# Performance work log

Measured on AMD Instinct MI355X. Metric: run time of the kernel, lower is better.

The kernel has to match this reference:

```python
import jax, jax.numpy as jnp
import numpy as np

NEG_SLOPE = 0.01  # torch LeakyReLU default
MIN_FREQ = 1.0
MAX_FREQ = 10.0
W = 100
N_HIDDEN = 100
N_OBS = 64

def _leaky(x):
    return jnp.where(x >= 0, x, NEG_SLOPE * x)

def setup_inputs() -> dict:
    key = jax.random.key(0)
    ks = jax.random.split(key, 7)
    # kaiming_uniform-ish init scales (exact init doesn't matter for correctness baseline)
    def unif(k, shape, fan_in):
        bound = np.sqrt(6.0 / fan_in)
        return jax.random.uniform(k, shape, jnp.float32, -bound, bound)
    x = jax.random.normal(ks[0], (65536, N_OBS), jnp.float32)
    W_in = unif(ks[1], (N_OBS, W), N_OBS)
    b_in = jnp.zeros((W,), jnp.float32)
    Ws = unif(ks[2], (N_HIDDEN, W, W), W)
    bs = jnp.zeros((N_HIDDEN, W), jnp.float32)
    W_out = unif(ks[3], (W, 1), W)
    b_out = jnp.zeros((1,), jnp.float32)
    return {"x": x, "W_in": W_in, "b_in": b_in, "Ws": Ws, "bs": bs,
            "W_out": W_out, "b_out": b_out}

def reference(x, W_in, b_in, Ws, bs, W_out, b_out):
    h = _leaky(x @ W_in + b_in)                       # [B, 100]
    def layer(h, wb):
        w, b = wb
        return _leaky(h @ w + b), None
    h, _ = jax.lax.scan(layer, h, (Ws, bs))           # 100 hidden layers
    a = h @ W_out + b_out                             # [B, 1]
    a = jnp.tanh(a)
    return (a + 1.0) / 2.0 * (MAX_FREQ - MIN_FREQ) + MIN_FREQ
```

## Files before the change

### kernel.cpp

```cpp
#include <hip/hip_runtime.h>
#include <cmath>

#define NLAYERS 100
#define DIN     64
#define WDIM    100
#define NTT     8
#define NTW     4
#define RT      4
#define ROWS    64
#define PSTR    136
#define RTPLANE (16 * PSTR)
#define BUF     (RT * RTPLANE)

typedef _Float16 half8 __attribute__((ext_vector_type(8)));
typedef _Float16 half2v __attribute__((ext_vector_type(2)));
typedef __fp16   fp16x2 __attribute__((ext_vector_type(2)));
typedef float    f32x4 __attribute__((ext_vector_type(4)));

#define WSH_LAYER_HALVES (4 * NTT * 64 * 8)
#define WSH_HALVES       (NLAYERS * WSH_LAYER_HALVES)
#define W0_HALVES        (2 * NTT * 64 * 8)
#define BPAD_FLOATS      128
#define OFF_BPAD_B       ((WSH_HALVES + W0_HALVES) * 2)
#define OFF_WOUT_B       (OFF_BPAD_B + BPAD_FLOATS * 4)
#define WOUT_FLOATS      128
#define TOTAL_PREP       (WSH_HALVES + W0_HALVES + BPAD_FLOATS + WOUT_FLOATS)

__global__ void actor_prep(const float* __restrict__ Win, const float* __restrict__ bin,
                           const float* __restrict__ Ws,  const float* __restrict__ bs,
                           const float* __restrict__ Wout,
                           _Float16* __restrict__ wsh, _Float16* __restrict__ w0sh,
                           float* __restrict__ bpad, float* __restrict__ woutp) {
    int t = blockIdx.x * 256 + threadIdx.x;
    if (t < WSH_HALVES) {
        int j    = t & 7;
        int lane = (t >> 3) & 63;
        int fid  = t >> 9;
        int nt   = fid & 7;
        int r2   = fid >> 3;
        int ks   = r2 & 3;
        int l    = r2 >> 2;
        int k = ks * 32 + (lane >> 4) * 8 + j;
        int n = nt * 16 + (lane & 15);
        float v = 0.f;
        if (k < WDIM && n < WDIM)            v = Ws[(l * WDIM + k) * WDIM + n];
        else if (k == 112 && n < WDIM)       v = bs[l * WDIM + n];
        else if (k == 112 && n == 112)       v = 1.0f;
        wsh[t] = (_Float16)v;
        return;
    }
    int t2 = t - WSH_HALVES;
    if (t2 < W0_HALVES) {
        int j    = t2 & 7;
        int lane = (t2 >> 3) & 63;
        int fid  = t2 >> 9;
        int nt   = fid & 7;
        int ks   = fid >> 3;
        int k = ks * 32 + (lane >> 4) * 8 + j;
        int n = nt * 16 + (lane & 15);
        float v = (k < DIN && n < WDIM) ? Win[k * WDIM + n] : 0.f;
        w0sh[t2] = (_Float16)v;
        return;
    }
    int t3 = t2 - W0_HALVES;
    if (t3 < BPAD_FLOATS) {
        float v = (t3 < WDIM) ? bin[t3] : (t3 == 112 ? 1.0f : 0.f);
        bpad[t3] = v;
        return;
    }
    int t4 = t3 - BPAD_FLOATS;
    if (t4 < WOUT_FLOATS) woutp[t4] = (t4 < WDIM) ? Wout[t4] : 0.f;
}

__device__ __forceinline__ void split8(const float* __restrict__ p, half8& hi, half8& lo) {
    f32x4 u0 = *(const f32x4*)p;
    f32x4 u1 = *(const f32x4*)(p + 4);
    float v[8] = {u0[0], u0[1], u0[2], u0[3], u1[0], u1[1], u1[2], u1[3]};
#pragma unroll
    for (int e = 0; e < 8; e += 2) {
        fp16x2 h = __builtin_amdgcn_cvt_pkrtz(v[e], v[e + 1]);
        float r0 = v[e]     - (float)h[0];
        float r1 = v[e + 1] - (float)h[1];
        fp16x2 l = __builtin_amdgcn_cvt_pkrtz(r0, r1);
        hi[e] = (_Float16)h[0]; hi[e + 1] = (_Float16)h[1];
        lo[e] = (_Float16)l[0]; lo[e + 1] = (_Float16)l[1];
    }
}

__device__ __forceinline__ void ep_tile(const f32x4 a, _Float16* __restrict__ d) {
    half2v p01, p23;
    p01[0] = (_Float16)a[0]; p01[1] = (_Float16)a[1];
    p23[0] = (_Float16)a[2]; p23[1] = (_Float16)a[3];
    const half2v slope = {(_Float16)0.01f, (_Float16)0.01f};
    p01 = __builtin_elementwise_max(p01, p01 * slope);
    p23 = __builtin_elementwise_max(p23, p23 * slope);
    uint2 w;
    w.x = __builtin_bit_cast(unsigned, p01);
    w.y = __builtin_bit_cast(unsigned, p23);
    *reinterpret_cast<uint2*>(d) = w;
}

__global__ __launch_bounds__(128, 2)
void actor_main(const float* __restrict__ x,
                const _Float16* __restrict__ wsh,
                const _Float16* __restrict__ w0sh,
                const float* __restrict__ bpad,
                const float* __restrict__ woutp,
                const float* __restrict__ bout,
                float* __restrict__ out) {
    __shared__ _Float16 hp[2 * BUF];
    const int lane = threadIdx.x & 63;
    const int wid  = threadIdx.x >> 6;
    const int q = lane >> 4, l15 = lane & 15;
    const int rowbase = blockIdx.x * ROWS;
    const int ntb = wid * NTW;

    f32x4 acc[RT][NTW];
    half8 wb[4][NTW];
    const f32x4 zero4 = {0.f, 0.f, 0.f, 0.f};

#pragma unroll
    for (int ks = 0; ks < 2; ++ks)
#pragma unroll
        for (int ntl = 0; ntl < NTW; ++ntl)
            wb[ks][ntl] = *(const half8*)(w0sh + (ks * NTT + ntb + ntl) * 512 + lane * 8);
#pragma unroll
    for (int rt = 0; rt < RT; ++rt)
#pragma unroll
        for (int ntl = 0; ntl < NTW; ++ntl)
            acc[rt][ntl] = *(const f32x4*)(bpad + (ntb + ntl) * 16 + q * 4);
#pragma unroll
    for (int rt = 0; rt < RT; ++rt) {
        const float* xr = x + (rowbase + rt * 16 + l15) * DIN;
#pragma unroll
        for (int ks = 0; ks < 2; ++ks) {
            half8 xhi, xlo;
            split8(xr + ks * 32 + q * 8, xhi, xlo);
#pragma unroll
            for (int ntl = 0; ntl < NTW; ++ntl) {
                acc[rt][ntl] = __builtin_amdgcn_mfma_f32_16x16x32_f16(wb[ks][ntl], xhi, acc[rt][ntl], 0, 0, 0);
                acc[rt][ntl] = __builtin_amdgcn_mfma_f32_16x16x32_f16(wb[ks][ntl], xlo, acc[rt][ntl], 0, 0, 0);
            }
        }
    }
#pragma unroll
    for (int rt = 0; rt < RT; ++rt)
#pragma unroll
        for (int ntl = 0; ntl < NTW; ++ntl)
            ep_tile(acc[rt][ntl], hp + rt * RTPLANE + l15 * PSTR + (ntb + ntl) * 16 + q * 4);
#pragma unroll
    for (int ks = 0; ks < 4; ++ks)
#pragma unroll
        for (int ntl = 0; ntl < NTW; ++ntl)
            wb[ks][ntl] = *(const half8*)(wsh + (ks * NTT + ntb + ntl) * 512 + lane * 8);
    __syncthreads();

#pragma unroll 1
    for (int l = 0; l < NLAYERS; ++l) {
        const _Float16* rb = hp + (l & 1) * BUF;
        _Float16* wbf = hp + ((l + 1) & 1) * BUF;
        const _Float16* wn = wsh + (l < NLAYERS - 1 ? l + 1 : l) * WSH_LAYER_HALVES;

#pragma unroll
        for (int rt = 0; rt < RT; ++rt) {
            half8 bh[4];
#pragma unroll
            for (int ks = 0; ks < 4; ++ks)
                bh[ks] = *(const half8*)(rb + rt * RTPLANE + l15 * PSTR + ks * 32 + q * 8);
            _Float16* dprev = wbf + (rt - 1) * RTPLANE + l15 * PSTR + q * 4;
#pragma unroll
            for (int ks = 0; ks < 4; ++ks) {
#pragma unroll
                for (int ntl = 0; ntl < NTW; ++ntl)
                    acc[rt][ntl] = __builtin_amdgcn_mfma_f32_16x16x32_f16(
                        wb[ks][ntl], bh[ks], (ks == 0 ? zero4 : acc[rt][ntl]), 0, 0, 0);
                if (rt >= 1)
                    ep_tile(acc[rt - 1][ks], dprev + (ntb + ks) * 16);
                if (rt == RT - 1) {
#pragma unroll
                    for (int ntl = 0; ntl < NTW; ++ntl)
                        wb[ks][ntl] = *(const half8*)(wn + (ks * NTT + ntb + ntl) * 512 + lane * 8);
                }
            }
        }
        _Float16* dlast = wbf + (RT - 1) * RTPLANE + l15 * PSTR + q * 4;
#pragma unroll
        for (int ntl = 0; ntl < NTW; ++ntl)
            ep_tile(acc[RT - 1][ntl], dlast + (ntb + ntl) * 16);
        __syncthreads();
    }

    float part[RT];
#pragma unroll
    for (int rt = 0; rt < RT; ++rt) {
        float s = 0.f;
#pragma unroll
        for (int ntl = 0; ntl < NTW; ++ntl) {
            f32x4 w4 = *(const f32x4*)(woutp + (ntb + ntl) * 16 + q * 4);
#pragma unroll
            for (int r = 0; r < 4; ++r) {
                float a = acc[rt][ntl][r];
                float v = fmaxf(a, 0.01f * a);
                s += v * w4[r];
            }
        }
        s += __shfl_xor(s, 16);
        s += __shfl_xor(s, 32);
        part[rt] = s;
    }
    float* red = (float*)hp;
#pragma unroll
    for (int rt = 0; rt < RT; ++rt)
        if (q == 0) red[wid * 64 + rt * 16 + l15] = part[rt];
    __syncthreads();
    {
        const int r = threadIdx.x;
        if (r < 64) {
            float tot = red[r] + red[64 + r] + bout[0];
            out[rowbase + r] = tanhf(tot) * 4.5f + 5.5f;
        }
    }
}

extern "C" void kernel_launch(void* const* d_in, const int* in_sizes, int n_in,
                              void* d_out, int out_size, void* d_ws, size_t ws_size,
                              hipStream_t stream) {
    const float* x    = (const float*)d_in[0];
    const float* Win  = (const float*)d_in[1];
    const float* bin  = (const float*)d_in[2];
    const float* Ws   = (const float*)d_in[3];
    const float* bs   = (const float*)d_in[4];
    const float* Wout = (const float*)d_in[5];
    const float* bout = (const float*)d_in[6];
    float* out = (float*)d_out;

    char* ws = (char*)d_ws;
    _Float16* wsh  = (_Float16*)ws;
    _Float16* w0sh = wsh + WSH_HALVES;
    float* bpad  = (float*)(ws + OFF_BPAD_B);
    float* woutp = (float*)(ws + OFF_WOUT_B);

    hipLaunchKernelGGL(actor_prep, dim3((TOTAL_PREP + 255) / 256), dim3(256), 0, stream,
                       Win, bin, Ws, bs, Wout, wsh, w0sh, bpad, woutp);

    const int nrows = in_sizes[0] / DIN;
    hipLaunchKernelGGL(actor_main, dim3(nrows / ROWS), dim3(128), 0, stream,
                       x, wsh, w0sh, bpad, woutp, bout, out);
}
```

Before: 262.9 us.

## Switch MLP layers to 32x32x16 MFMA tiles with K padded to 112

```diff
diff --git a/kernel.cpp b/kernel.cpp
--- a/kernel.cpp
+++ b/kernel.cpp
@@ -4,22 +4,23 @@
 #define NLAYERS 100
 #define DIN     64
 #define WDIM    100
-#define NTT     8
-#define NTW     4
-#define RT      4
+#define NTT     4
+#define NTW     2
+#define RT      2
 #define ROWS    64
+#define KS      7
 #define PSTR    136
-#define RTPLANE (16 * PSTR)
-#define BUF     (RT * RTPLANE)
-
-typedef _Float16 half8 __attribute__((ext_vector_type(8)));
+#define BUF     (64 * PSTR)
+
+typedef _Float16 half8  __attribute__((ext_vector_type(8)));
 typedef _Float16 half2v __attribute__((ext_vector_type(2)));
 typedef __fp16   fp16x2 __attribute__((ext_vector_type(2)));
-typedef float    f32x4 __attribute__((ext_vector_type(4)));
-
-#define WSH_LAYER_HALVES (4 * NTT * 64 * 8)
+typedef float    f32x4  __attribute__((ext_vector_type(4)));
+typedef float    f32x16 __attribute__((ext_vector_type(16)));
+
+#define WSH_LAYER_HALVES (KS * NTT * 64 * 8)
 #define WSH_HALVES       (NLAYERS * WSH_LAYER_HALVES)
-#define W0_HALVES        (2 * NTT * 64 * 8)
+#define W0_HALVES        (4 * NTT * 64 * 8)
 #define BPAD_FLOATS      128
 #define OFF_BPAD_B       ((WSH_HALVES + W0_HALVES) * 2)
 #define OFF_WOUT_B       (OFF_BPAD_B + BPAD_FLOATS * 4)
@@ -36,16 +37,16 @@
         int j    = t & 7;
         int lane = (t >> 3) & 63;
         int fid  = t >> 9;
-        int nt   = fid & 7;
-        int r2   = fid >> 3;
-        int ks   = r2 & 3;
-        int l    = r2 >> 2;
-        int k = ks * 32 + (lane >> 4) * 8 + j;
-        int n = nt * 16 + (lane & 15);
+        int nt   = fid & 3;
+        int r2   = fid >> 2;
+        int ks   = r2 % 7;
+        int l    = r2 / 7;
+        int k = ks * 16 + (lane >> 5) * 8 + j;
+        int n = nt * 32 + (lane & 31);
         float v = 0.f;
         if (k < WDIM && n < WDIM)            v = Ws[(l * WDIM + k) * WDIM + n];
-        else if (k == 112 && n < WDIM)       v = bs[l * WDIM + n];
-        else if (k == 112 && n == 112)       v = 1.0f;
+        else if (k == 100 && n < WDIM)       v = bs[l * WDIM + n];
+        else if (k == 100 && n == 100)       v = 1.0f;
         wsh[t] = (_Float16)v;
         return;
     }
@@ -54,17 +55,17 @@
         int j    = t2 & 7;
         int lane = (t2 >> 3) & 63;
         int fid  = t2 >> 9;
-        int nt   = fid & 7;
-        int ks   = fid >> 3;
-        int k = ks * 32 + (lane >> 4) * 8 + j;
-        int n = nt * 16 + (lane & 15);
-        float v = (k < DIN && n < WDIM) ? Win[k * WDIM + n] : 0.f;
+        int nt   = fid & 3;
+        int ks   = fid >> 2;
+        int k = ks * 16 + (lane >> 5) * 8 + j;
+        int n = nt * 32 + (lane & 31);
+        float v = (n < WDIM) ? Win[k * WDIM + n] : 0.f;
         w0sh[t2] = (_Float16)v;
         return;
     }
     int t3 = t2 - W0_HALVES;
     if (t3 < BPAD_FLOATS) {
-        float v = (t3 < WDIM) ? bin[t3] : (t3 == 112 ? 1.0f : 0.f);
+        float v = (t3 < WDIM) ? bin[t3] : (t3 == 100 ? 1.0f : 0.f);
         bpad[t3] = v;
         return;
     }
@@ -87,10 +88,10 @@
     }
 }
 
-__device__ __forceinline__ void ep_tile(const f32x4 a, _Float16* __restrict__ d) {
+__device__ __forceinline__ void ep_quad(const f32x16 a, int qd, _Float16* __restrict__ d) {
     half2v p01, p23;
-    p01[0] = (_Float16)a[0]; p01[1] = (_Float16)a[1];
-    p23[0] = (_Float16)a[2]; p23[1] = (_Float16)a[3];
+    p01[0] = (_Float16)a[4 * qd + 0]; p01[1] = (_Float16)a[4 * qd + 1];
+    p23[0] = (_Float16)a[4 * qd + 2]; p23[1] = (_Float16)a[4 * qd + 3];
     const half2v slope = {(_Float16)0.01f, (_Float16)0.01f};
     p01 = __builtin_elementwise_max(p01, p01 * slope);
     p23 = __builtin_elementwise_max(p23, p23 * slope);
@@ -111,45 +112,54 @@
     __shared__ _Float16 hp[2 * BUF];
     const int lane = threadIdx.x & 63;
     const int wid  = threadIdx.x >> 6;
-    const int q = lane >> 4, l15 = lane & 15;
+    const int g = lane >> 5, b31 = lane & 31;
     const int rowbase = blockIdx.x * ROWS;
     const int ntb = wid * NTW;
 
-    f32x4 acc[RT][NTW];
-    half8 wb[4][NTW];
-    const f32x4 zero4 = {0.f, 0.f, 0.f, 0.f};
-
-#pragma unroll
-    for (int ks = 0; ks < 2; ++ks)
-#pragma unroll
-        for (int ntl = 0; ntl < NTW; ++ntl)
-            wb[ks][ntl] = *(const half8*)(w0sh + (ks * NTT + ntb + ntl) * 512 + lane * 8);
+    f32x16 acc[RT][NTW];
+    half8 wb[KS][NTW];
+    const f32x16 zero16 = {0,0,0,0, 0,0,0,0, 0,0,0,0, 0,0,0,0};
+
+    half8 w0[4][NTW];
+#pragma unroll
+    for (int ks = 0; ks < 4; ++ks)
+#pragma unroll
+        for (int ntl = 0; ntl < NTW; ++ntl)
+            w0[ks][ntl] = *(const half8*)(w0sh + (ks * NTT + ntb + ntl) * 512 + lane * 8);
 #pragma unroll
     for (int rt = 0; rt < RT; ++rt)
 #pragma unroll
         for (int ntl = 0; ntl < NTW; ++ntl)
-            acc[rt][ntl] = *(const f32x4*)(bpad + (ntb + ntl) * 16 + q * 4);
+#pragma unroll
+            for (int qd = 0; qd < 4; ++qd) {
+                f32x4 tq = *(const f32x4*)(bpad + (ntb + ntl) * 32 + 8 * qd + 4 * g);
+#pragma unroll
+                for (int r = 0; r < 4; ++r) acc[rt][ntl][4 * qd + r] = tq[r];
+            }
 #pragma unroll
     for (int rt = 0; rt < RT; ++rt) {
-        const float* xr = x + (rowbase + rt * 16 + l15) * DIN;
-#pragma unroll
-        for (int ks = 0; ks < 2; ++ks) {
+        const float* xr = x + (rowbase + rt * 32 + b31) * DIN;
+#pragma unroll
+        for (int ks = 0; ks < 4; ++ks) {
             half8 xhi, xlo;
-            split8(xr + ks * 32 + q * 8, xhi, xlo);
+            split8(xr + ks * 16 + g * 8, xhi, xlo);
 #pragma unroll
             for (int ntl = 0; ntl < NTW; ++ntl) {
-                acc[rt][ntl] = __builtin_amdgcn_mfma_f32_16x16x32_f16(wb[ks][ntl], xhi, acc[rt][ntl], 0, 0, 0);
-                acc[rt][ntl] = __builtin_amdgcn_mfma_f32_16x16x32_f16(wb[ks][ntl], xlo, acc[rt][ntl], 0, 0, 0);
+                acc[rt][ntl] = __builtin_amdgcn_mfma_f32_32x32x16_f16(w0[ks][ntl], xhi, acc[rt][ntl], 0, 0, 0);
+                acc[rt][ntl] = __builtin_amdgcn_mfma_f32_32x32x16_f16(w0[ks][ntl], xlo, acc[rt][ntl], 0, 0, 0);
             }
         }
     }
 #pragma unroll
     for (int rt = 0; rt < RT; ++rt)
 #pragma unroll
-        for (int ntl = 0; ntl < NTW; ++ntl)
-            ep_tile(acc[rt][ntl], hp + rt * RTPLANE + l15 * PSTR + (ntb + ntl) * 16 + q * 4);
-#pragma unroll
-    for (int ks = 0; ks < 4; ++ks)
+        for (int ntl = 0; ntl < NTW; ++ntl) {
+            _Float16* d = hp + (rt * 32 + b31) * PSTR + (ntb + ntl) * 32 + 4 * g;
+#pragma unroll
+            for (int qd = 0; qd < 4; ++qd) ep_quad(acc[rt][ntl], qd, d + 8 * qd);
+        }
+#pragma unroll
+    for (int ks = 0; ks < KS; ++ks)
 #pragma unroll
         for (int ntl = 0; ntl < NTW; ++ntl)
             wb[ks][ntl] = *(const half8*)(wsh + (ks * NTT + ntb + ntl) * 512 + lane * 8);
@@ -160,33 +170,35 @@
         const _Float16* rb = hp + (l & 1) * BUF;
         _Float16* wbf = hp + ((l + 1) & 1) * BUF;
         const _Float16* wn = wsh + (l < NLAYERS - 1 ? l + 1 : l) * WSH_LAYER_HALVES;
-
-#pragma unroll
-        for (int rt = 0; rt < RT; ++rt) {
-            half8 bh[4];
-#pragma unroll
-            for (int ks = 0; ks < 4; ++ks)
-                bh[ks] = *(const half8*)(rb + rt * RTPLANE + l15 * PSTR + ks * 32 + q * 8);
-            _Float16* dprev = wbf + (rt - 1) * RTPLANE + l15 * PSTR + q * 4;
-#pragma unroll
-            for (int ks = 0; ks < 4; ++ks) {
-#pragma unroll
-                for (int ntl = 0; ntl < NTW; ++ntl)
-                    acc[rt][ntl] = __builtin_amdgcn_mfma_f32_16x16x32_f16(
-                        wb[ks][ntl], bh[ks], (ks == 0 ? zero4 : acc[rt][ntl]), 0, 0, 0);
-                if (rt >= 1)
-                    ep_tile(acc[rt - 1][ks], dprev + (ntb + ks) * 16);
-                if (rt == RT - 1) {
-#pragma unroll
-                    for (int ntl = 0; ntl < NTW; ++ntl)
-                        wb[ks][ntl] = *(const half8*)(wn + (ks * NTT + ntb + ntl) * 512 + lane * 8);
-                }
-            }
-        }
-        _Float16* dlast = wbf + (RT - 1) * RTPLANE + l15 * PSTR + q * 4;
-#pragma unroll
-        for (int ntl = 0; ntl < NTW; ++ntl)
-            ep_tile(acc[RT - 1][ntl], dlast + (ntb + ntl) * 16);
+        half8 bh[KS];
+
+#pragma unroll
+        for (int c = 0; c < 4; ++c) {
+            const int rt = c >> 1, ntl = c & 1;
+            if (ntl == 0) {
+#pragma unroll
+                for (int ks = 0; ks < KS; ++ks)
+                    bh[ks] = *(const half8*)(rb + (rt * 32 + b31) * PSTR + ks * 16 + g * 8);
+            }
+            const int prt = (c - 1) >> 1, pntl = (c - 1) & 1;
+            _Float16* dp = wbf + (prt * 32 + b31) * PSTR + (ntb + pntl) * 32 + 4 * g;
+#pragma unroll
+            for (int ks = 0; ks < KS; ++ks) {
+                acc[rt][ntl] = __builtin_amdgcn_mfma_f32_32x32x16_f16(
+                    wb[ks][ntl], bh[ks], (ks == 0 ? zero16 : acc[rt][ntl]), 0, 0, 0);
+                if (c > 0 && ks < 4)
+                    ep_quad(acc[prt][pntl], ks, dp + 8 * ks);
+                if (c == 2)
+                    wb[ks][0] = *(const half8*)(wn + (ks * NTT + ntb + 0) * 512 + lane * 8);
+                if (c == 3)
+                    wb[ks][1] = *(const half8*)(wn + (ks * NTT + ntb + 1) * 512 + lane * 8);
+            }
+        }
+        {
+            _Float16* dl = wbf + (32 + b31) * PSTR + (ntb + 1) * 32 + 4 * g;
+#pragma unroll
+            for (int qd = 0; qd < 4; ++qd) ep_quad(acc[1][1], qd, dl + 8 * qd);
+        }
         __syncthreads();
     }
 
@@ -195,23 +207,24 @@
     for (int rt = 0; rt < RT; ++rt) {
         float s = 0.f;
 #pragma unroll
-        for (int ntl = 0; ntl < NTW; ++ntl) {
-            f32x4 w4 = *(const f32x4*)(woutp + (ntb + ntl) * 16 + q * 4);
-#pragma unroll
-            for (int r = 0; r < 4; ++r) {
-                float a = acc[rt][ntl][r];
-                float v = fmaxf(a, 0.01f * a);
-                s += v * w4[r];
-            }
-        }
-        s += __shfl_xor(s, 16);
+        for (int ntl = 0; ntl < NTW; ++ntl)
+#pragma unroll
+            for (int qd = 0; qd < 4; ++qd) {
+                f32x4 w4 = *(const f32x4*)(woutp + (ntb + ntl) * 32 + 8 * qd + 4 * g);
+#pragma unroll
+                for (int r = 0; r < 4; ++r) {
+                    float a = acc[rt][ntl][4 * qd + r];
+                    float v = fmaxf(a, 0.01f * a);
+                    s += v * w4[r];
+                }
+            }
         s += __shfl_xor(s, 32);
         part[rt] = s;
     }
     float* red = (float*)hp;
 #pragma unroll
     for (int rt = 0; rt < RT; ++rt)
-        if (q == 0) red[wid * 64 + rt * 16 + l15] = part[rt];
+        if (lane < 32) red[wid * 64 + rt * 32 + b31] = part[rt];
     __syncthreads();
     {
         const int r = threadIdx.x;
```

Measured after the change: 264.8 us. Within noise of the previous version (+0.7%).
